# Optimization experiments

Measured on AMD Instinct MI355X. Metric: run time of the kernel, lower is better.

Reference implementation:

```python
import jax, jax.numpy as jnp
import numpy as np

NUM_HEADS = 16
HEAD_DIM = 64
HIDDEN = NUM_HEADS * HEAD_DIM  # 1024
SEQ_LEN = 4096


def setup_inputs() -> dict:
    key = jax.random.key(0)
    ks = jax.random.split(key, 8)
    hidden_states = jax.random.normal(ks[0], (SEQ_LEN, HIDDEN), dtype=jnp.float32)
    cu_seqlens = jnp.sort(jax.random.randint(ks[1], (5,), 0, SEQ_LEN)).astype(jnp.int32)
    cos = jax.random.uniform(ks[2], (SEQ_LEN, HEAD_DIM), dtype=jnp.float32)
    sin = jax.random.uniform(ks[3], (SEQ_LEN, HEAD_DIM), dtype=jnp.float32)
    W_qkv = jax.random.normal(ks[4], (HIDDEN, 3 * HIDDEN), dtype=jnp.float32) * 0.02
    b_qkv = jax.random.normal(ks[5], (3 * HIDDEN,), dtype=jnp.float32) * 0.02
    W_proj = jax.random.normal(ks[6], (HIDDEN, HIDDEN), dtype=jnp.float32) * 0.02
    b_proj = jax.random.normal(ks[7], (HIDDEN,), dtype=jnp.float32) * 0.02
    return {
        "hidden_states": hidden_states,
        "cu_seqlens": cu_seqlens,
        "cos": cos,
        "sin": sin,
        "W_qkv": W_qkv,
        "b_qkv": b_qkv,
        "W_proj": W_proj,
        "b_proj": b_proj,
    }


def _rotate_half(x):
    x1, x2 = jnp.split(x, 2, axis=-1)
    return jnp.concatenate([-x2, x1], axis=-1)


def reference(hidden_states, cu_seqlens, cos, sin, W_qkv, b_qkv, W_proj, b_proj):
    # NOTE: original module does not use cu_seqlens for masking (full dense attention).
    seq_len = hidden_states.shape[0]
    qkv = hidden_states @ W_qkv + b_qkv  # (S, 3*H)
    qkv = qkv.reshape(seq_len, 3, NUM_HEADS, HEAD_DIM)
    q, k, v = qkv[:, 0], qkv[:, 1], qkv[:, 2]  # (S, nh, hd)
    c = cos[:, None, :]
    s = sin[:, None, :]
    q = q * c + _rotate_half(q) * s
    k = k * c + _rotate_half(k) * s
    scale = 1.0 / jnp.sqrt(jnp.float32(HEAD_DIM))
    # (nh, S, hd)
    q = q.transpose(1, 0, 2)
    k = k.transpose(1, 0, 2)
    v = v.transpose(1, 0, 2)
    attn = jnp.einsum('hqd,hkd->hqk', q, k) * scale
    attn = jax.nn.softmax(attn, axis=-1)
    out = jnp.einsum('hqk,hkd->hqd', attn, v)
    out = out.transpose(1, 0, 2).reshape(seq_len, HIDDEN)
    return out @ W_proj + b_proj
```

## Files before the change

### kernel.cpp

```cpp
#include <hip/hip_runtime.h>
#include <type_traits>

typedef short bf16x8 __attribute__((ext_vector_type(8)));
typedef float f32x4  __attribute__((ext_vector_type(4)));
typedef unsigned short u16;

#define MFMA(a,b,c) __builtin_amdgcn_mfma_f32_16x16x32_bf16((a),(b),(c),0,0,0)

__device__ __forceinline__ float bf2f(u16 u){ unsigned x=((unsigned)u)<<16; return __builtin_bit_cast(float,x); }
__device__ __forceinline__ u16 f2bf(float f){ unsigned x=__builtin_bit_cast(unsigned,f); x += 0x7fffu + ((x>>16)&1u); return (u16)(x>>16); }

#if __has_builtin(__builtin_amdgcn_cvt_pk_bf16_f32)
typedef __bf16 hwbf2 __attribute__((ext_vector_type(2)));
__device__ __forceinline__ unsigned pkbf(float a, float b){
  hwbf2 r = __builtin_amdgcn_cvt_pk_bf16_f32(a, b);
  return __builtin_bit_cast(unsigned, r);
}
#else
__device__ __forceinline__ unsigned pkbf(float a, float b){
  unsigned ua = __builtin_bit_cast(unsigned, a), ub = __builtin_bit_cast(unsigned, b);
  ua += 0x7fffu + ((ua>>16)&1u);
  ub += 0x7fffu + ((ub>>16)&1u);
  return __builtin_amdgcn_perm(ub, ua, 0x07060302u);
}
#endif

#if __has_builtin(__builtin_amdgcn_exp2f)
#define EXP2(x) __builtin_amdgcn_exp2f(x)
#else
#define EXP2(x) exp2f(x)
#endif

__device__ __forceinline__ void async_cp16(const u16* g, u16* l){
  __builtin_amdgcn_global_load_lds((const __attribute__((address_space(1))) void*)g,
                                   (__attribute__((address_space(3))) void*)l, 16, 0, 0);
}

__global__ __launch_bounds__(256) void cvt_f32_bf16(const float* __restrict__ in, u16* __restrict__ out, int n){
  int i = (blockIdx.x*256 + threadIdx.x)*4;
  if (i >= n) return;
  float4 v = *(const float4*)(in + i);
  ushort4 o;
  o.x = f2bf(v.x); o.y = f2bf(v.y); o.z = f2bf(v.z); o.w = f2bf(v.w);
  *(ushort4*)(out + i) = o;
}

__global__ __launch_bounds__(256) void transpose_f32_bf16(const float* __restrict__ in, u16* __restrict__ out, int R, int C){
  __shared__ u16 tile[32][33];
  int bc = blockIdx.x*32, br = blockIdx.y*32;
  int tx = threadIdx.x & 31, ty = threadIdx.x >> 5;
  #pragma unroll
  for (int i=ty;i<32;i+=8) tile[i][tx] = f2bf(in[(size_t)(br+i)*C + bc + tx]);
  __syncthreads();
  #pragma unroll
  for (int i=ty;i<32;i+=8) out[(size_t)(bc+i)*R + br + tx] = tile[tx][i];
}

__global__ __launch_bounds__(256) void vtrans_perm_bf16(const u16* __restrict__ in, u16* __restrict__ out){
  __shared__ u16 tile[32][33];
  const int h = blockIdx.z;
  const u16* ip = in + (size_t)h*4096*64;
  u16* op = out + (size_t)h*64*4096;
  int bt = blockIdx.x*32, bd = blockIdx.y*32;
  int tx = threadIdx.x & 31, ty = threadIdx.x >> 5;
  #pragma unroll
  for (int i=ty;i<32;i+=8) tile[i][tx] = ip[(size_t)(bt+i)*64 + bd + tx];
  __syncthreads();
  const int tlog = ((tx>>2)&1)*16 + (tx>>3)*4 + (tx&3);
  #pragma unroll
  for (int i=ty;i<32;i+=8) op[(size_t)(bd+i)*4096 + bt + tx] = tile[tlog][i];
}

template<int BN, typename OutT>
__global__ __launch_bounds__(256) void gemm_bt_bias(
    const u16* __restrict__ A, const u16* __restrict__ Bt,
    const float* __restrict__ bias, OutT* __restrict__ C,
    int M, int N, int K)
{
  __shared__ __align__(16) u16 As[128*32];
  __shared__ __align__(16) u16 Bs[BN*32];
  const int m0 = blockIdx.y*128, n0 = blockIdx.x*BN;
  const int tid = threadIdx.x;
  const int wave = tid>>6, lane = tid&63;
  const int wr = (wave>>1)*64, wc = (wave&1)*(BN/2);
  const int ml = lane&15, quad = lane>>4;
  const int lrow = lane>>2;
  const int scol = ((lane&3) ^ (lrow&3))*8;
  const int rsw  = (quad ^ (ml&3))*8;
  const u16* gA0 = A + (size_t)(m0 + wave*32      + lrow)*K + scol;
  const u16* gA1 = A + (size_t)(m0 + wave*32 + 16 + lrow)*K + scol;
  u16* lA0 = &As[wave*1024];
  u16* lA1 = &As[wave*1024 + 512];
  constexpr int BI = BN/64;
  const u16* gB[BI]; u16* lB[BI];
  #pragma unroll
  for (int t=0;t<BI;t++){
    gB[t] = Bt + (size_t)(n0 + (wave*BI+t)*16 + lrow)*K + scol;
    lB[t] = &Bs[(wave*BI+t)*512];
  }
  constexpr int NJ = BN/32;
  f32x4 acc[4][NJ] = {};
  for (int k0=0; k0<K; k0+=32) {
    async_cp16(gA0 + k0, lA0);
    async_cp16(gA1 + k0, lA1);
    #pragma unroll
    for (int t=0;t<BI;t++) async_cp16(gB[t] + k0, lB[t]);
    __syncthreads();
    bf16x8 af[4], bfr[NJ];
    #pragma unroll
    for (int i=0;i<4;i++)  af[i]  = *(const bf16x8*)&As[(wr+i*16+ml)*32 + rsw];
    #pragma unroll
    for (int j=0;j<NJ;j++) bfr[j] = *(const bf16x8*)&Bs[(wc+j*16+ml)*32 + rsw];
    #pragma unroll
    for (int i=0;i<4;i++)
      #pragma unroll
      for (int j=0;j<NJ;j++)
        acc[i][j] = MFMA(af[i], bfr[j], acc[i][j]);
    __syncthreads();
  }
  #pragma unroll
  for (int j=0;j<NJ;j++){
    int col = n0 + wc + j*16 + ml;
    float bv = bias[col];
    #pragma unroll
    for (int i=0;i<4;i++){
      int row0 = m0 + wr + i*16 + quad*4;
      #pragma unroll
      for (int r=0;r<4;r++){
        float val = acc[i][j][r] + bv;
        if constexpr (std::is_same_v<OutT, float>)
          C[(size_t)(row0+r)*N + col] = val;
        else
          C[(size_t)(row0+r)*N + col] = f2bf(val);
      }
    }
  }
}

__global__ __launch_bounds__(256) void rope_split(
    const u16* __restrict__ QKV, const float* __restrict__ cosb, const float* __restrict__ sinb,
    u16* __restrict__ Qo, u16* __restrict__ Ko, u16* __restrict__ Vo)
{
  const int t = blockIdx.x;
  const int d = threadIdx.x & 63;
  const int h0 = threadIdx.x >> 6;
  const float cv = cosb[t*64+d];
  const float sv = sinb[t*64+d];
  const int dp = (d<32) ? d+32 : d-32;
  const float sgn = (d<32) ? -1.f : 1.f;
  #pragma unroll
  for (int h=h0; h<16; h+=4) {
    const u16* base = QKV + (size_t)t*3072 + h*64;
    float q  = bf2f(base[d]);
    float k  = bf2f(base[1024+d]);
    float v  = bf2f(base[2048+d]);
    float qp = bf2f(base[dp]);
    float kp = bf2f(base[1024+dp]);
    float qr = q*cv + sgn*qp*sv;
    float kr = k*cv + sgn*kp*sv;
    Qo[((size_t)h*4096 + t)*64 + d] = f2bf(qr*(0.125f*1.44269504f));
    Ko[((size_t)h*4096 + t)*64 + d] = f2bf(kr);
    Vo[((size_t)h*4096 + t)*64 + d] = f2bf(v);
  }
}

__global__ __launch_bounds__(256,4) void flash_attn(
    const u16* __restrict__ Q, const u16* __restrict__ Kg, const u16* __restrict__ VT,
    u16* __restrict__ O0, u16* __restrict__ O1, u16* __restrict__ O2, u16* __restrict__ O3,
    float* __restrict__ Lpart)
{
  constexpr int SEQ=4096, QTR=1024;
  __shared__ __align__(16) u16 Ks[64*64];
  __shared__ __align__(16) u16 Vs[64*64];
  const int qt=blockIdx.x, h=blockIdx.y, ks=blockIdx.z;
  const int tid=threadIdx.x, wave=tid>>6, lane=tid&63;
  const int ml=lane&15, quad=lane>>4;
  const int qbase = qt*128 + wave*32;
  bf16x8 qf[2][2];
  #pragma unroll
  for (int qi=0; qi<2; qi++){
    const u16* qp = Q + ((size_t)h*SEQ + qbase + qi*16 + ml)*64;
    qf[qi][0] = *(const bf16x8*)(qp + quad*8);
    qf[qi][1] = *(const bf16x8*)(qp + 32 + quad*8);
  }
  const bf16x8 ones = {0x3F80,0x3F80,0x3F80,0x3F80,0x3F80,0x3F80,0x3F80,0x3F80};
  f32x4 o[2][4] = {};
  f32x4 accsum[2] = {};
  const int lrow8 = lane>>3, lchk = lane&7;
  const int swzg = (lchk ^ lrow8)*8;
  const u16* kgl = Kg + (size_t)h*SEQ*64 + (size_t)(ks*QTR + wave*16 + lrow8)*64 + swzg;
  const u16* vgl = VT + (size_t)h*64*SEQ + (size_t)(wave*16 + lrow8)*SEQ + ks*QTR + swzg;
  u16* kl0 = &Ks[(wave*16  )*64];
  u16* kl1 = &Ks[(wave*16+8)*64];
  u16* vl0 = &Vs[(wave*16  )*64];
  u16* vl1 = &Vs[(wave*16+8)*64];
  const int swzA = (quad     ^ (ml&7))*8;
  const int swzB = ((quad^4) ^ (ml&7))*8;

  for (int k0=0;k0<QTR;k0+=64) {
    async_cp16(kgl + (size_t)k0*64,       kl0);
    async_cp16(kgl + (size_t)k0*64 + 512, kl1);
    async_cp16(vgl + k0,                  vl0);
    async_cp16(vgl + 8*SEQ + k0,          vl1);
    __syncthreads();
    f32x4 s[2][4];
    #pragma unroll
    for (int kb=0;kb<4;kb++){
      bf16x8 kf0 = *(const bf16x8*)&Ks[(kb*16+ml)*64 + swzA];
      bf16x8 kf1 = *(const bf16x8*)&Ks[(kb*16+ml)*64 + swzB];
      f32x4 z0={0,0,0,0}, z1={0,0,0,0};
      z0 = MFMA(kf0, qf[0][0], z0); s[0][kb] = MFMA(kf1, qf[0][1], z0);
      z1 = MFMA(kf0, qf[1][0], z1); s[1][kb] = MFMA(kf1, qf[1][1], z1);
    }
    bf16x8 vf[4][2];
    #pragma unroll
    for (int db=0;db<4;db++){
      vf[db][0] = *(const bf16x8*)&Vs[(db*16+ml)*64 + swzA];
      vf[db][1] = *(const bf16x8*)&Vs[(db*16+ml)*64 + swzB];
    }
    #pragma unroll
    for (int qi=0; qi<2; qi++)
      #pragma unroll
      for (int p=0;p<2;p++){
        float e0 = EXP2(s[qi][2*p][0]),   e1 = EXP2(s[qi][2*p][1]);
        float e2 = EXP2(s[qi][2*p][2]),   e3 = EXP2(s[qi][2*p][3]);
        float e4 = EXP2(s[qi][2*p+1][0]), e5 = EXP2(s[qi][2*p+1][1]);
        float e6 = EXP2(s[qi][2*p+1][2]), e7 = EXP2(s[qi][2*p+1][3]);
        union { uint4 u; bf16x8 v; } pf;
        pf.u.x = pkbf(e0,e1); pf.u.y = pkbf(e2,e3);
        pf.u.z = pkbf(e4,e5); pf.u.w = pkbf(e6,e7);
        accsum[qi] = MFMA(ones, pf.v, accsum[qi]);
        #pragma unroll
        for (int db=0;db<4;db++)
          o[qi][db] = MFMA(vf[db][p], pf.v, o[qi][db]);
      }
    __syncthreads();
  }
  u16* op = (ks==0) ? O0 : (ks==1) ? O1 : (ks==2) ? O2 : O3;
  #pragma unroll
  for (int qi=0;qi<2;qi++){
    size_t rb = (size_t)(qbase + qi*16 + ml)*1024 + h*64;
    #pragma unroll
    for (int db=0;db<4;db++){
      uint2 w;
      w.x = pkbf(o[qi][db][0], o[qi][db][1]);
      w.y = pkbf(o[qi][db][2], o[qi][db][3]);
      *(uint2*)&op[rb + db*16 + quad*4] = w;
    }
  }
  if (quad==0){
    float* lp = Lpart + (size_t)ks*65536 + (size_t)h*4096 + qbase;
    lp[ml]    = accsum[0][0];
    lp[16+ml] = accsum[1][0];
  }
}

__global__ __launch_bounds__(256) void combine_softmax4(
    const u16* __restrict__ O0, const u16* __restrict__ O1,
    const u16* __restrict__ O2, const u16* __restrict__ O3,
    const float* __restrict__ L, u16* __restrict__ AO)
{
  int i = (blockIdx.x*256 + threadIdx.x)*4;
  int row = i >> 10, col = i & 1023, h = col >> 6;
  int li = h*4096 + row;
  float inv = 1.f/(L[li] + L[li+65536] + L[li+2*65536] + L[li+3*65536]);
  ushort4 a = *(const ushort4*)(O0+i);
  ushort4 b = *(const ushort4*)(O1+i);
  ushort4 c = *(const ushort4*)(O2+i);
  ushort4 d = *(const ushort4*)(O3+i);
  ushort4 o;
  o.x = f2bf((bf2f(a.x)+bf2f(b.x)+bf2f(c.x)+bf2f(d.x))*inv);
  o.y = f2bf((bf2f(a.y)+bf2f(b.y)+bf2f(c.y)+bf2f(d.y))*inv);
  o.z = f2bf((bf2f(a.z)+bf2f(b.z)+bf2f(c.z)+bf2f(d.z))*inv);
  o.w = f2bf((bf2f(a.w)+bf2f(b.w)+bf2f(c.w)+bf2f(d.w))*inv);
  *(ushort4*)(AO+i) = o;
}

extern "C" void kernel_launch(void* const* d_in, const int* in_sizes, int n_in,
                              void* d_out, int out_size, void* d_ws, size_t ws_size,
                              hipStream_t stream)
{
  (void)in_sizes; (void)n_in; (void)out_size; (void)ws_size;
  const float* H     = (const float*)d_in[0];
  const float* cosb  = (const float*)d_in[2];
  const float* sinb  = (const float*)d_in[3];
  const float* Wqkv  = (const float*)d_in[4];
  const float* bqkv  = (const float*)d_in[5];
  const float* Wproj = (const float*)d_in[6];
  const float* bproj = (const float*)d_in[7];
  float* out = (float*)d_out;
  char* ws = (char*)d_ws;
  float* Lpart  = (float*)(ws + 0);
  u16*   WprojT = (u16*)(ws + 2097152);
  u16*   Hb     = (u16*)(ws + 4194304);
  u16*   Opart2 = (u16*)(ws + 4194304);
  u16*   QKVr   = (u16*)(ws + 12582912);
  u16*   VTb    = (u16*)(ws + 12582912);
  u16*   Opart0 = (u16*)(ws + 20971520);
  u16*   Opart1 = (u16*)(ws + 29360128);
  u16*   WqkvT  = (u16*)(ws + 37748736);
  u16*   Qb     = (u16*)(ws + 37748736);
  u16*   AO     = (u16*)(ws + 37748736);
  u16*   Kb     = (u16*)(ws + 46137344);
  u16*   Vb     = (u16*)(ws + 54525952);
  u16*   Opart3 = (u16*)(ws + 54525952);

  hipLaunchKernelGGL(cvt_f32_bf16, dim3(4096), dim3(256), 0, stream, H, Hb, 4096*1024);
  hipLaunchKernelGGL(transpose_f32_bf16, dim3(96,32), dim3(256), 0, stream, Wqkv, WqkvT, 1024, 3072);
  hipLaunchKernelGGL(transpose_f32_bf16, dim3(32,32), dim3(256), 0, stream, Wproj, WprojT, 1024, 1024);
  hipLaunchKernelGGL((gemm_bt_bias<128,u16>), dim3(24,32), dim3(256), 0, stream, Hb, WqkvT, bqkv, QKVr, 4096, 3072, 1024);
  hipLaunchKernelGGL(rope_split, dim3(4096), dim3(256), 0, stream, QKVr, cosb, sinb, Qb, Kb, Vb);
  hipLaunchKernelGGL(vtrans_perm_bf16, dim3(128,2,16), dim3(256), 0, stream, Vb, VTb);
  hipLaunchKernelGGL(flash_attn, dim3(32,16,4), dim3(256), 0, stream, Qb, Kb, VTb,
                     Opart0, Opart1, Opart2, Opart3, Lpart);
  hipLaunchKernelGGL(combine_softmax4, dim3(4096), dim3(256), 0, stream,
                     Opart0, Opart1, Opart2, Opart3, Lpart, AO);
  hipLaunchKernelGGL((gemm_bt_bias<64,float>), dim3(16,32), dim3(256), 0, stream, AO, WprojT, bproj, out, 4096, 1024, 1024);
}
```

Measured before the change: 256.3 us.

## Fuse RoPE with V transpose, deepen GEMM K-tile, enlarge flash-attn query tile

```diff
diff --git a/kernel.cpp b/kernel.cpp
--- a/kernel.cpp
+++ b/kernel.cpp
@@ -56,66 +56,57 @@
   for (int i=ty;i<32;i+=8) out[(size_t)(bc+i)*R + br + tx] = tile[tx][i];
 }
 
-__global__ __launch_bounds__(256) void vtrans_perm_bf16(const u16* __restrict__ in, u16* __restrict__ out){
-  __shared__ u16 tile[32][33];
-  const int h = blockIdx.z;
-  const u16* ip = in + (size_t)h*4096*64;
-  u16* op = out + (size_t)h*64*4096;
-  int bt = blockIdx.x*32, bd = blockIdx.y*32;
-  int tx = threadIdx.x & 31, ty = threadIdx.x >> 5;
-  #pragma unroll
-  for (int i=ty;i<32;i+=8) tile[i][tx] = ip[(size_t)(bt+i)*64 + bd + tx];
-  __syncthreads();
-  const int tlog = ((tx>>2)&1)*16 + (tx>>3)*4 + (tx&3);
-  #pragma unroll
-  for (int i=ty;i<32;i+=8) op[(size_t)(bd+i)*4096 + bt + tx] = tile[tlog][i];
-}
-
 template<int BN, typename OutT>
 __global__ __launch_bounds__(256) void gemm_bt_bias(
     const u16* __restrict__ A, const u16* __restrict__ Bt,
     const float* __restrict__ bias, OutT* __restrict__ C,
     int M, int N, int K)
 {
-  __shared__ __align__(16) u16 As[128*32];
-  __shared__ __align__(16) u16 Bs[BN*32];
+  __shared__ __align__(16) u16 As[128*64];
+  __shared__ __align__(16) u16 Bs[BN*64];
   const int m0 = blockIdx.y*128, n0 = blockIdx.x*BN;
-  const int tid = threadIdx.x;
-  const int wave = tid>>6, lane = tid&63;
+  const int tid = threadIdx.x, wave = tid>>6, lane = tid&63;
   const int wr = (wave>>1)*64, wc = (wave&1)*(BN/2);
   const int ml = lane&15, quad = lane>>4;
-  const int lrow = lane>>2;
-  const int scol = ((lane&3) ^ (lrow&3))*8;
-  const int rsw  = (quad ^ (ml&3))*8;
-  const u16* gA0 = A + (size_t)(m0 + wave*32      + lrow)*K + scol;
-  const u16* gA1 = A + (size_t)(m0 + wave*32 + 16 + lrow)*K + scol;
-  u16* lA0 = &As[wave*1024];
-  u16* lA1 = &As[wave*1024 + 512];
-  constexpr int BI = BN/64;
+  const int lrow8 = lane>>3, lchk = lane&7;
+  const int swzg = (lchk ^ lrow8)*8;
+  const u16* gA[4]; u16* lA[4];
+  #pragma unroll
+  for (int t=0;t<4;t++){
+    gA[t] = A + (size_t)(m0 + wave*32 + t*8 + lrow8)*K + swzg;
+    lA[t] = &As[(wave*32 + t*8)*64];
+  }
+  constexpr int BI = BN/32;
   const u16* gB[BI]; u16* lB[BI];
   #pragma unroll
   for (int t=0;t<BI;t++){
-    gB[t] = Bt + (size_t)(n0 + (wave*BI+t)*16 + lrow)*K + scol;
-    lB[t] = &Bs[(wave*BI+t)*512];
+    gB[t] = Bt + (size_t)(n0 + wave*(BN/4) + t*8 + lrow8)*K + swzg;
+    lB[t] = &Bs[(wave*(BN/4) + t*8)*64];
   }
   constexpr int NJ = BN/32;
   f32x4 acc[4][NJ] = {};
-  for (int k0=0; k0<K; k0+=32) {
-    async_cp16(gA0 + k0, lA0);
-    async_cp16(gA1 + k0, lA1);
-    #pragma unroll
-    for (int t=0;t<BI;t++) async_cp16(gB[t] + k0, lB[t]);
+  const int rch0 = ( quad      ^ (ml&7))*8;
+  const int rch1 = ((quad|4) ^ (ml&7))*8;
+  for (int k0=0; k0<K; k0+=64) {
+    #pragma unroll
+    for (int t=0;t<4;t++)  async_cp16(gA[t]+k0, lA[t]);
+    #pragma unroll
+    for (int t=0;t<BI;t++) async_cp16(gB[t]+k0, lB[t]);
     __syncthreads();
-    bf16x8 af[4], bfr[NJ];
-    #pragma unroll
-    for (int i=0;i<4;i++)  af[i]  = *(const bf16x8*)&As[(wr+i*16+ml)*32 + rsw];
-    #pragma unroll
-    for (int j=0;j<NJ;j++) bfr[j] = *(const bf16x8*)&Bs[(wc+j*16+ml)*32 + rsw];
-    #pragma unroll
-    for (int i=0;i<4;i++)
-      #pragma unroll
-      for (int j=0;j<NJ;j++)
-        acc[i][j] = MFMA(af[i], bfr[j], acc[i][j]);
+    #pragma unroll
+    for (int kk=0;kk<2;kk++){
+      const int rc = kk ? rch1 : rch0;
+      bf16x8 af[4], bfr[NJ];
+      #pragma unroll
+      for (int i=0;i<4;i++)  af[i]  = *(const bf16x8*)&As[(wr+i*16+ml)*64 + rc];
+      #pragma unroll
+      for (int j=0;j<NJ;j++) bfr[j] = *(const bf16x8*)&Bs[(wc+j*16+ml)*64 + rc];
+      #pragma unroll
+      for (int i=0;i<4;i++)
+        #pragma unroll
+        for (int j=0;j<NJ;j++)
+          acc[i][j] = MFMA(af[i], bfr[j], acc[i][j]);
+    }
     __syncthreads();
   }
   #pragma unroll
@@ -137,34 +128,66 @@
   }
 }
 
-__global__ __launch_bounds__(256) void rope_split(
+__global__ __launch_bounds__(256) void rope_split_vt(
     const u16* __restrict__ QKV, const float* __restrict__ cosb, const float* __restrict__ sinb,
-    u16* __restrict__ Qo, u16* __restrict__ Ko, u16* __restrict__ Vo)
-{
-  const int t = blockIdx.x;
-  const int d = threadIdx.x & 63;
-  const int h0 = threadIdx.x >> 6;
-  const float cv = cosb[t*64+d];
-  const float sv = sinb[t*64+d];
-  const int dp = (d<32) ? d+32 : d-32;
-  const float sgn = (d<32) ? -1.f : 1.f;
-  #pragma unroll
-  for (int h=h0; h<16; h+=4) {
-    const u16* base = QKV + (size_t)t*3072 + h*64;
-    float q  = bf2f(base[d]);
-    float k  = bf2f(base[1024+d]);
-    float v  = bf2f(base[2048+d]);
-    float qp = bf2f(base[dp]);
-    float kp = bf2f(base[1024+dp]);
-    float qr = q*cv + sgn*qp*sv;
-    float kr = k*cv + sgn*kp*sv;
-    Qo[((size_t)h*4096 + t)*64 + d] = f2bf(qr*(0.125f*1.44269504f));
-    Ko[((size_t)h*4096 + t)*64 + d] = f2bf(kr);
-    Vo[((size_t)h*4096 + t)*64 + d] = f2bf(v);
-  }
-}
-
-__global__ __launch_bounds__(256,4) void flash_attn(
+    u16* __restrict__ Qo, u16* __restrict__ Ko, u16* __restrict__ VTo)
+{
+  __shared__ __align__(16) u16 vt[64*40];
+  const int t0 = blockIdx.x*32, h = blockIdx.y;
+  const int tid = threadIdx.x;
+  const int tl = tid>>3, d8 = (tid&7)*8;
+  const int t = t0 + tl;
+  const u16* base = QKV + (size_t)t*3072 + h*64 + d8;
+  uint4 qw = *(const uint4*)base;
+  uint4 kw = *(const uint4*)(base + 1024);
+  uint4 vw = *(const uint4*)(base + 2048);
+  uint4 qp, kp;
+  qp.x=__shfl_xor((int)qw.x,4,64); qp.y=__shfl_xor((int)qw.y,4,64);
+  qp.z=__shfl_xor((int)qw.z,4,64); qp.w=__shfl_xor((int)qw.w,4,64);
+  kp.x=__shfl_xor((int)kw.x,4,64); kp.y=__shfl_xor((int)kw.y,4,64);
+  kp.z=__shfl_xor((int)kw.z,4,64); kp.w=__shfl_xor((int)kw.w,4,64);
+  const float* cp = cosb + (size_t)t*64 + d8;
+  const float* sp = sinb + (size_t)t*64 + d8;
+  float4 c0 = *(const float4*)cp, c1 = *(const float4*)(cp+4);
+  float4 s0 = *(const float4*)sp, s1 = *(const float4*)(sp+4);
+  const float sgn = (d8<32) ? -1.f : 1.f;
+  const unsigned* qwa = &qw.x; const unsigned* qpa = &qp.x;
+  const unsigned* kwa = &kw.x; const unsigned* kpa = &kp.x;
+  const float* ca = &c0.x; const float* sa = &s0.x;
+  float cc[8] = {c0.x,c0.y,c0.z,c0.w,c1.x,c1.y,c1.z,c1.w};
+  float ss[8] = {s0.x,s0.y,s0.z,s0.w,s1.x,s1.y,s1.z,s1.w};
+  (void)ca; (void)sa;
+  unsigned qout[4], kout[4];
+  #pragma unroll
+  for (int p=0;p<4;p++){
+    u16 qa = (u16)(qwa[p]&0xffff), qb = (u16)(qwa[p]>>16);
+    u16 pa = (u16)(qpa[p]&0xffff), pb = (u16)(qpa[p]>>16);
+    float r0 = bf2f(qa)*cc[2*p]   + sgn*bf2f(pa)*ss[2*p];
+    float r1 = bf2f(qb)*cc[2*p+1] + sgn*bf2f(pb)*ss[2*p+1];
+    qout[p] = pkbf(r0*(0.125f*1.44269504f), r1*(0.125f*1.44269504f));
+    u16 ka_ = (u16)(kwa[p]&0xffff), kb_ = (u16)(kwa[p]>>16);
+    u16 pka = (u16)(kpa[p]&0xffff), pkb2 = (u16)(kpa[p]>>16);
+    float k0_ = bf2f(ka_)*cc[2*p]   + sgn*bf2f(pka)*ss[2*p];
+    float k1_ = bf2f(kb_)*cc[2*p+1] + sgn*bf2f(pkb2)*ss[2*p+1];
+    kout[p] = pkbf(k0_, k1_);
+  }
+  size_t qkrow = ((size_t)h*4096 + t)*64 + d8;
+  *(uint4*)&Qo[qkrow] = *(uint4*)qout;
+  *(uint4*)&Ko[qkrow] = *(uint4*)kout;
+  const int tph = ((tl>>2)&3)*8 + ((tl>>4)&1)*4 + (tl&3);
+  const unsigned* vwa = &vw.x;
+  #pragma unroll
+  for (int p=0;p<4;p++){
+    vt[(d8+2*p  )*40 + tph] = (u16)(vwa[p]&0xffff);
+    vt[(d8+2*p+1)*40 + tph] = (u16)(vwa[p]>>16);
+  }
+  __syncthreads();
+  const int d_out = tid>>2, t8 = (tid&3)*8;
+  uint4 w = *(const uint4*)&vt[d_out*40 + t8];
+  *(uint4*)&VTo[((size_t)h*64 + d_out)*4096 + t0 + t8] = w;
+}
+
+__global__ __launch_bounds__(256,2) void flash_attn(
     const u16* __restrict__ Q, const u16* __restrict__ Kg, const u16* __restrict__ VT,
     u16* __restrict__ O0, u16* __restrict__ O1, u16* __restrict__ O2, u16* __restrict__ O3,
     float* __restrict__ Lpart)
@@ -175,17 +198,17 @@
   const int qt=blockIdx.x, h=blockIdx.y, ks=blockIdx.z;
   const int tid=threadIdx.x, wave=tid>>6, lane=tid&63;
   const int ml=lane&15, quad=lane>>4;
-  const int qbase = qt*128 + wave*32;
-  bf16x8 qf[2][2];
-  #pragma unroll
-  for (int qi=0; qi<2; qi++){
+  const int qbase = qt*256 + wave*64;
+  bf16x8 qf[4][2];
+  #pragma unroll
+  for (int qi=0; qi<4; qi++){
     const u16* qp = Q + ((size_t)h*SEQ + qbase + qi*16 + ml)*64;
     qf[qi][0] = *(const bf16x8*)(qp + quad*8);
     qf[qi][1] = *(const bf16x8*)(qp + 32 + quad*8);
   }
   const bf16x8 ones = {0x3F80,0x3F80,0x3F80,0x3F80,0x3F80,0x3F80,0x3F80,0x3F80};
-  f32x4 o[2][4] = {};
-  f32x4 accsum[2] = {};
+  f32x4 o[4][4] = {};
+  f32x4 accsum[4] = {};
   const int lrow8 = lane>>3, lchk = lane&7;
   const int swzg = (lchk ^ lrow8)*8;
   const u16* kgl = Kg + (size_t)h*SEQ*64 + (size_t)(ks*QTR + wave*16 + lrow8)*64 + swzg;
@@ -194,7 +217,7 @@
   u16* kl1 = &Ks[(wave*16+8)*64];
   u16* vl0 = &Vs[(wave*16  )*64];
   u16* vl1 = &Vs[(wave*16+8)*64];
-  const int swzA = (quad     ^ (ml&7))*8;
+  const int swzA = ( quad     ^ (ml&7))*8;
   const int swzB = ((quad^4) ^ (ml&7))*8;
 
   for (int k0=0;k0<QTR;k0+=64) {
@@ -203,14 +226,17 @@
     async_cp16(vgl + k0,                  vl0);
     async_cp16(vgl + 8*SEQ + k0,          vl1);
     __syncthreads();
-    f32x4 s[2][4];
+    f32x4 s[4][4];
     #pragma unroll
     for (int kb=0;kb<4;kb++){
       bf16x8 kf0 = *(const bf16x8*)&Ks[(kb*16+ml)*64 + swzA];
       bf16x8 kf1 = *(const bf16x8*)&Ks[(kb*16+ml)*64 + swzB];
-      f32x4 z0={0,0,0,0}, z1={0,0,0,0};
-      z0 = MFMA(kf0, qf[0][0], z0); s[0][kb] = MFMA(kf1, qf[0][1], z0);
-      z1 = MFMA(kf0, qf[1][0], z1); s[1][kb] = MFMA(kf1, qf[1][1], z1);
+      #pragma unroll
+      for (int qi=0;qi<4;qi++){
+        f32x4 z = {0,0,0,0};
+        z = MFMA(kf0, qf[qi][0], z);
+        s[qi][kb] = MFMA(kf1, qf[qi][1], z);
+      }
     }
     bf16x8 vf[4][2];
     #pragma unroll
@@ -219,7 +245,7 @@
       vf[db][1] = *(const bf16x8*)&Vs[(db*16+ml)*64 + swzB];
     }
     #pragma unroll
-    for (int qi=0; qi<2; qi++)
+    for (int qi=0; qi<4; qi++)
       #pragma unroll
       for (int p=0;p<2;p++){
         float e0 = EXP2(s[qi][2*p][0]),   e1 = EXP2(s[qi][2*p][1]);
@@ -238,7 +264,7 @@
   }
   u16* op = (ks==0) ? O0 : (ks==1) ? O1 : (ks==2) ? O2 : O3;
   #pragma unroll
-  for (int qi=0;qi<2;qi++){
+  for (int qi=0;qi<4;qi++){
     size_t rb = (size_t)(qbase + qi*16 + ml)*1024 + h*64;
     #pragma unroll
     for (int db=0;db<4;db++){
@@ -250,8 +276,8 @@
   }
   if (quad==0){
     float* lp = Lpart + (size_t)ks*65536 + (size_t)h*4096 + qbase;
-    lp[ml]    = accsum[0][0];
-    lp[16+ml] = accsum[1][0];
+    #pragma unroll
+    for (int qi=0;qi<4;qi++) lp[qi*16+ml] = accsum[qi][0];
   }
 }
 
@@ -293,25 +319,23 @@
   float* Lpart  = (float*)(ws + 0);
   u16*   WprojT = (u16*)(ws + 2097152);
   u16*   Hb     = (u16*)(ws + 4194304);
-  u16*   Opart2 = (u16*)(ws + 4194304);
+  u16*   VTb    = (u16*)(ws + 4194304);
   u16*   QKVr   = (u16*)(ws + 12582912);
-  u16*   VTb    = (u16*)(ws + 12582912);
-  u16*   Opart0 = (u16*)(ws + 20971520);
-  u16*   Opart1 = (u16*)(ws + 29360128);
+  u16*   Opart0 = (u16*)(ws + 12582912);
+  u16*   Opart1 = (u16*)(ws + 20971520);
+  u16*   Opart2 = (u16*)(ws + 29360128);
   u16*   WqkvT  = (u16*)(ws + 37748736);
   u16*   Qb     = (u16*)(ws + 37748736);
   u16*   AO     = (u16*)(ws + 37748736);
   u16*   Kb     = (u16*)(ws + 46137344);
-  u16*   Vb     = (u16*)(ws + 54525952);
   u16*   Opart3 = (u16*)(ws + 54525952);
 
   hipLaunchKernelGGL(cvt_f32_bf16, dim3(4096), dim3(256), 0, stream, H, Hb, 4096*1024);
   hipLaunchKernelGGL(transpose_f32_bf16, dim3(96,32), dim3(256), 0, stream, Wqkv, WqkvT, 1024, 3072);
   hipLaunchKernelGGL(transpose_f32_bf16, dim3(32,32), dim3(256), 0, stream, Wproj, WprojT, 1024, 1024);
   hipLaunchKernelGGL((gemm_bt_bias<128,u16>), dim3(24,32), dim3(256), 0, stream, Hb, WqkvT, bqkv, QKVr, 4096, 3072, 1024);
-  hipLaunchKernelGGL(rope_split, dim3(4096), dim3(256), 0, stream, QKVr, cosb, sinb, Qb, Kb, Vb);
-  hipLaunchKernelGGL(vtrans_perm_bf16, dim3(128,2,16), dim3(256), 0, stream, Vb, VTb);
-  hipLaunchKernelGGL(flash_attn, dim3(32,16,4), dim3(256), 0, stream, Qb, Kb, VTb,
+  hipLaunchKernelGGL(rope_split_vt, dim3(128,16), dim3(256), 0, stream, QKVr, cosb, sinb, Qb, Kb, VTb);
+  hipLaunchKernelGGL(flash_attn, dim3(16,16,4), dim3(256), 0, stream, Qb, Kb, VTb,
                      Opart0, Opart1, Opart2, Opart3, Lpart);
   hipLaunchKernelGGL(combine_softmax4, dim3(4096), dim3(256), 0, stream,
                      Opart0, Opart1, Opart2, Opart3, Lpart, AO);
```

Result: no change. 256.9 us (+0.2%).
